# Performance work log

Hardware: AMD Instinct MI355X
Metric: run time of the kernel (lower is better)

The kernel has to match this reference:

```python
import jax, jax.numpy as jnp
import numpy as np

N = 4096
IN_F = 512
OUT_F = 256
HEADS = 4
HEAD_DIM = OUT_F // HEADS


def setup_inputs() -> dict:
    key = jax.random.key(0)
    k_feat, k_adj, k_w, k_a = jax.random.split(key, 4)
    features = jax.random.normal(k_feat, (N, IN_F), dtype=jnp.float32)
    adj_matrix = jax.random.uniform(k_adj, (N, N), dtype=jnp.float32)
    # xavier-uniform-ish init scaled small
    W = jax.random.normal(k_w, (OUT_F, IN_F), dtype=jnp.float32) * (1.0 / np.sqrt(IN_F))
    a = jax.random.normal(k_a, (HEADS, 2 * HEAD_DIM), dtype=jnp.float32) * 0.1
    bias = jnp.zeros((OUT_F,), dtype=jnp.float32)
    return {"features": features, "adj_matrix": adj_matrix, "W": W, "a": a, "bias": bias}


def reference(features, adj_matrix, W, a, bias):
    n = features.shape[0]
    h = features @ W.T                      # [N, OUT_F]
    hh = h.reshape(n, HEADS, HEAD_DIM)      # [N, H, D]
    # e[i,j,h] = leaky_relu(<h_i, a[:, :D]> + <h_j, a[:, D:]>) -- additive decomposition
    e_src = jnp.einsum('nhd,hd->nh', hh, a[:, :HEAD_DIM])   # [N, H]
    e_dst = jnp.einsum('nhd,hd->nh', hh, a[:, HEAD_DIM:])   # [N, H]
    e = e_src[:, None, :] + e_dst[None, :, :]               # [N, N, H]
    e = jnp.where(e >= 0, e, 0.2 * e)                       # leaky_relu(0.2)
    mask = adj_matrix[:, :, None] > 0.1                     # [N, N, 1]
    e = jnp.where(mask, e, -jnp.inf)
    attention = jax.nn.softmax(e, axis=1)                   # softmax over j
    attention = jnp.nan_to_num(attention, nan=0.0)          # fully-masked rows -> 0
    attention_mean = attention.mean(axis=2)                 # [N, N]
    h_out = attention_mean @ h + bias                       # [N, OUT_F]
    return h_out
```

## Files before the change

### kernel.cpp

```cpp
#include <hip/hip_runtime.h>
#include <math.h>

#define NN      4096
#define INF_    512
#define OUTF    256
#define NHEAD   4
#define HDIM    64
#define KSPLIT  8

typedef __attribute__((ext_vector_type(8))) short  short8x;
typedef __attribute__((ext_vector_type(4))) float  float4x;
typedef __attribute__((ext_vector_type(2))) float  float2x;

__device__ __forceinline__ unsigned short f2bf(float x) {
    union { float f; unsigned int u; } c; c.f = x;
    unsigned int r = (c.u + 0x7FFFu + ((c.u >> 16) & 1u)) >> 16;
    return (unsigned short)r;
}
__device__ __forceinline__ float2x bf2up(unsigned int u) {
    union { unsigned int x; float f; } lo, hi;
    lo.x = u << 16; hi.x = u & 0xFFFF0000u;
    float2x r; r[0] = lo.f; r[1] = hi.f; return r;
}
__device__ __forceinline__ float2x max2(float2x a, float2x b) {
    float2x r; r[0] = fmaxf(a[0], b[0]); r[1] = fmaxf(a[1], b[1]); return r;
}

__global__ __launch_bounds__(256) void k_cast(const float* __restrict__ feat,
                                              const float* __restrict__ W,
                                              unsigned short* __restrict__ featb,
                                              unsigned short* __restrict__ Wb) {
    const int b = blockIdx.x;
    const float* src;
    unsigned short* dst;
    int idx;
    if (b < 2048) { src = feat; dst = featb; idx = b * 1024 + threadIdx.x * 4; }
    else          { src = W;    dst = Wb;    idx = (b - 2048) * 1024 + threadIdx.x * 4; }
    float4x v = *(const float4x*)(src + idx);
    ushort4 u;
    u.x = f2bf(v[0]); u.y = f2bf(v[1]); u.z = f2bf(v[2]); u.w = f2bf(v[3]);
    *(ushort4*)(dst + idx) = u;
}

__global__ __launch_bounds__(256) void k_hedge(const unsigned short* __restrict__ featb,
                                               const unsigned short* __restrict__ Wb,
                                               const float* __restrict__ a,
                                               unsigned short* __restrict__ hT,
                                               float* __restrict__ es,
                                               unsigned short* __restrict__ Bt,
                                               unsigned short* __restrict__ Dt) {
    __shared__ __align__(16) unsigned short lds_f[64 * 40];
    __shared__ __align__(16) unsigned short lds_w[256 * 40];
    const int tid  = threadIdx.x;
    const int w    = tid >> 6;
    const int lane = tid & 63;
    const int lidx = lane & 15;
    const int quad = lane >> 4;
    const int i0   = blockIdx.x * 64;
    const int sr = tid >> 2;
    const int skq = (tid & 3) * 8;

    float4x acc[4][4];
    #pragma unroll
    for (int p = 0; p < 4; ++p)
        #pragma unroll
        for (int q = 0; q < 4; ++q)
            acc[p][q] = (float4x){0.f, 0.f, 0.f, 0.f};

    for (int kt = 0; kt < INF_; kt += 32) {
        __syncthreads();
        *(ushort4*)&lds_f[sr * 40 + skq]     = *(const ushort4*)&featb[(size_t)(i0 + sr) * INF_ + kt + skq];
        *(ushort4*)&lds_f[sr * 40 + skq + 4] = *(const ushort4*)&featb[(size_t)(i0 + sr) * INF_ + kt + skq + 4];
        #pragma unroll
        for (int itr = 0; itr < 4; ++itr) {
            int n = itr * 64 + sr;
            *(ushort4*)&lds_w[n * 40 + skq]     = *(const ushort4*)&Wb[(size_t)n * INF_ + kt + skq];
            *(ushort4*)&lds_w[n * 40 + skq + 4] = *(const ushort4*)&Wb[(size_t)n * INF_ + kt + skq + 4];
        }
        __syncthreads();
        short8x af[4], bw[4];
        #pragma unroll
        for (int t = 0; t < 4; ++t) {
            af[t] = *(const short8x*)&lds_f[(t * 16 + lidx) * 40 + quad * 8];
            bw[t] = *(const short8x*)&lds_w[(w * 64 + t * 16 + lidx) * 40 + quad * 8];
        }
        #pragma unroll
        for (int it = 0; it < 4; ++it)
            #pragma unroll
            for (int nt = 0; nt < 4; ++nt)
                acc[it][nt] = __builtin_amdgcn_mfma_f32_16x16x32_bf16(
                    af[it], bw[nt], acc[it][nt], 0, 0, 0);
    }
    #pragma unroll
    for (int it = 0; it < 4; ++it)
        #pragma unroll
        for (int nt = 0; nt < 4; ++nt) {
            int col = w * 64 + nt * 16 + lidx;
            int m0r = i0 + it * 16 + quad * 4;
            ushort4 u;
            u.x = f2bf(acc[it][nt][0]); u.y = f2bf(acc[it][nt][1]);
            u.z = f2bf(acc[it][nt][2]); u.w = f2bf(acc[it][nt][3]);
            *(ushort4*)&hT[(size_t)col * NN + m0r] = u;
        }
    float asrc[4], adst[4];
    #pragma unroll
    for (int nt = 0; nt < 4; ++nt) {
        asrc[nt] = a[w * 2 * HDIM + nt * 16 + lidx];
        adst[nt] = a[w * 2 * HDIM + HDIM + nt * 16 + lidx];
    }
    #pragma unroll
    for (int it = 0; it < 4; ++it)
        #pragma unroll
        for (int r = 0; r < 4; ++r) {
            float s = 0.f, d = 0.f;
            #pragma unroll
            for (int nt = 0; nt < 4; ++nt) {
                s += acc[it][nt][r] * asrc[nt];
                d += acc[it][nt][r] * adst[nt];
            }
            #pragma unroll
            for (int off = 1; off < 16; off <<= 1) {
                s += __shfl_xor(s, off);
                d += __shfl_xor(d, off);
            }
            if (lidx == 0) {
                int row = i0 + it * 16 + quad * 4 + r;
                es[row * NHEAD + w] = s;
                Bt[row * NHEAD + w] = f2bf(__expf(d));
                Dt[row * NHEAD + w] = f2bf(__expf(0.2f * d));
            }
        }
}

__global__ __launch_bounds__(256) void k_attn(const float* __restrict__ adj,
                                              const float* __restrict__ es,
                                              const unsigned short* __restrict__ Bt,
                                              const unsigned short* __restrict__ Dt,
                                              unsigned short* __restrict__ attn) {
    __shared__ float red[4][4];
    __shared__ float cfs[4];
    const int tid = threadIdx.x;
    const int wv  = tid >> 6;
    const int lane = tid & 63;
    const int i = blockIdx.x;

    const float4x esv = ((const float4x*)es)[i];
    float2x A01, A23, C01, C23;
    A01[0] = __expf(esv[0]); A01[1] = __expf(esv[1]);
    A23[0] = __expf(esv[2]); A23[1] = __expf(esv[3]);
    C01[0] = __expf(0.2f * esv[0]); C01[1] = __expf(0.2f * esv[1]);
    C23[0] = __expf(0.2f * esv[2]); C23[1] = __expf(0.2f * esv[3]);

    const float4x* arow4 = (const float4x*)(adj + (size_t)i * NN);
    const uint4* B4 = (const uint4*)Bt;
    const uint4* D4 = (const uint4*)Dt;

    float2x m01[4][4], m23[4][4];
    float2x den01 = (float2x){0.f, 0.f};
    float2x den23 = (float2x){0.f, 0.f};
    #pragma unroll
    for (int t = 0; t < 4; ++t) {
        int jv = t * 256 + tid;
        float4x av = arow4[jv];
        uint4 bu0 = B4[jv * 2], bu1 = B4[jv * 2 + 1];
        uint4 du0 = D4[jv * 2], du1 = D4[jv * 2 + 1];
        unsigned int bwv[8] = {bu0.x, bu0.y, bu0.z, bu0.w, bu1.x, bu1.y, bu1.z, bu1.w};
        unsigned int dwv[8] = {du0.x, du0.y, du0.z, du0.w, du1.x, du1.y, du1.z, du1.w};
        #pragma unroll
        for (int u = 0; u < 4; ++u) {
            float2x b01 = bf2up(bwv[u * 2]);
            float2x b23 = bf2up(bwv[u * 2 + 1]);
            float2x d01 = bf2up(dwv[u * 2]);
            float2x d23 = bf2up(dwv[u * 2 + 1]);
            float mf = (av[u] > 0.1f) ? 1.f : 0.f;
            float2x mf2; mf2[0] = mf; mf2[1] = mf;
            m01[t][u] = mf2 * max2(A01 * b01, C01 * d01);
            m23[t][u] = mf2 * max2(A23 * b23, C23 * d23);
            den01 += m01[t][u];
            den23 += m23[t][u];
        }
    }
    float dh[4] = {den01[0], den01[1], den23[0], den23[1]};
    #pragma unroll
    for (int off = 1; off < 64; off <<= 1) {
        #pragma unroll
        for (int h = 0; h < 4; ++h)
            dh[h] += __shfl_xor(dh[h], off);
    }
    if (lane == 0) {
        #pragma unroll
        for (int h = 0; h < 4; ++h) red[wv][h] = dh[h];
    }
    __syncthreads();
    if (tid < 4)
        cfs[tid] = red[0][tid] + red[1][tid] + red[2][tid] + red[3][tid];
    __syncthreads();
    float sc[4];
    #pragma unroll
    for (int h = 0; h < 4; ++h) {
        float den = cfs[h];
        sc[h] = den > 0.f ? 0.25f / den : 0.f;
    }

    unsigned short* orow = attn + (size_t)i * NN;
    #pragma unroll
    for (int t = 0; t < 4; ++t) {
        int jv = t * 256 + tid;
        ushort4 o;
        unsigned short* op = (unsigned short*)&o;
        #pragma unroll
        for (int u = 0; u < 4; ++u) {
            float p = sc[0] * m01[t][u][0] + sc[1] * m01[t][u][1]
                    + sc[2] * m23[t][u][0] + sc[3] * m23[t][u][1];
            op[u] = f2bf(p);
        }
        *(ushort4*)&orow[jv * 4] = o;
    }
}

__global__ __launch_bounds__(256) void k_out_gemm(const unsigned short* __restrict__ attn,
                                                  const unsigned short* __restrict__ hT,
                                                  float* __restrict__ partials) {
    __shared__ __align__(16) unsigned short lds_a[32 * 40];
    __shared__ __align__(16) unsigned short lds_h[256 * 40];
    const int tid  = threadIdx.x;
    const int w    = tid >> 6;
    const int lane = tid & 63;
    const int lidx = lane & 15;
    const int quad = lane >> 4;
    const int i0    = blockIdx.x * 32;
    const int kbase = blockIdx.y * (NN / KSPLIT);
    const int srow = tid >> 3;
    const int skq  = tid & 7;

    float4x acc[2][4];
    #pragma unroll
    for (int p = 0; p < 2; ++p)
        #pragma unroll
        for (int q = 0; q < 4; ++q)
            acc[p][q] = (float4x){0.f, 0.f, 0.f, 0.f};

    ushort4 pa, ph[8];
    pa = *(const ushort4*)&attn[(size_t)(i0 + srow) * NN + kbase + skq * 4];
    #pragma unroll
    for (int it = 0; it < 8; ++it)
        ph[it] = *(const ushort4*)&hT[(size_t)(it * 32 + srow) * NN + kbase + skq * 4];

    const int KSTEPS = (NN / KSPLIT) / 32;
    for (int ks = 0; ks < KSTEPS; ++ks) {
        __syncthreads();
        *(ushort4*)&lds_a[srow * 40 + skq * 4] = pa;
        #pragma unroll
        for (int it = 0; it < 8; ++it)
            *(ushort4*)&lds_h[(it * 32 + srow) * 40 + skq * 4] = ph[it];
        __syncthreads();
        if (ks < KSTEPS - 1) {
            const int ktn = kbase + (ks + 1) * 32;
            pa = *(const ushort4*)&attn[(size_t)(i0 + srow) * NN + ktn + skq * 4];
            #pragma unroll
            for (int it = 0; it < 8; ++it)
                ph[it] = *(const ushort4*)&hT[(size_t)(it * 32 + srow) * NN + ktn + skq * 4];
        }
        short8x af[2], bfr[4];
        #pragma unroll
        for (int t = 0; t < 2; ++t)
            af[t]  = *(const short8x*)&lds_a[(t * 16 + lidx) * 40 + quad * 8];
        #pragma unroll
        for (int t = 0; t < 4; ++t)
            bfr[t] = *(const short8x*)&lds_h[(w * 64 + t * 16 + lidx) * 40 + quad * 8];
        #pragma unroll
        for (int it = 0; it < 2; ++it)
            #pragma unroll
            for (int nt = 0; nt < 4; ++nt)
                acc[it][nt] = __builtin_amdgcn_mfma_f32_16x16x32_bf16(
                    af[it], bfr[nt], acc[it][nt], 0, 0, 0);
    }
    float* pbase = partials + (size_t)blockIdx.y * NN * OUTF;
    #pragma unroll
    for (int it = 0; it < 2; ++it)
        #pragma unroll
        for (int nt = 0; nt < 4; ++nt)
            #pragma unroll
            for (int rr = 0; rr < 4; ++rr) {
                int row = i0 + it * 16 + quad * 4 + rr;
                int col = w * 64 + nt * 16 + lidx;
                pbase[(size_t)row * OUTF + col] = acc[it][nt][rr];
            }
}

__global__ __launch_bounds__(256) void k_reduce_out(const float* __restrict__ partials,
                                                    const float* __restrict__ bias,
                                                    float* __restrict__ out) {
    const int i = blockIdx.x;
    const int n = threadIdx.x;
    float acc = bias[n];
    #pragma unroll
    for (int s = 0; s < KSPLIT; ++s)
        acc += partials[((size_t)s * NN + i) * OUTF + n];
    out[(size_t)i * OUTF + n] = acc;
}

extern "C" void kernel_launch(void* const* d_in, const int* in_sizes, int n_in,
                              void* d_out, int out_size, void* d_ws, size_t ws_size,
                              hipStream_t stream) {
    const float* feat = (const float*)d_in[0];
    const float* adj  = (const float*)d_in[1];
    const float* W    = (const float*)d_in[2];
    const float* a    = (const float*)d_in[3];
    const float* bias = (const float*)d_in[4];
    float* out = (float*)d_out;

    char* ws = (char*)d_ws;
    float*          es    = (float*)(ws + 0);
    unsigned short* Btb   = (unsigned short*)(ws + (64u << 10));
    unsigned short* Dtb   = (unsigned short*)(ws + (96u << 10));
    unsigned short* hT    = (unsigned short*)(ws + (256u << 10));
    unsigned short* attn  = (unsigned short*)(ws + (2560u << 10));
    unsigned short* featb = (unsigned short*)(ws + (2560u << 10));
    unsigned short* Wb    = (unsigned short*)(ws + (6656u << 10));
    float*          partials = (float*)(ws + (35328u << 10));

    k_cast      <<<2176,              256, 0, stream>>>(feat, W, featb, Wb);
    k_hedge     <<<64,                256, 0, stream>>>(featb, Wb, a, hT, es, Btb, Dtb);
    k_attn      <<<NN,                256, 0, stream>>>(adj, es, Btb, Dtb, attn);
    k_out_gemm  <<<dim3(128, KSPLIT), 256, 0, stream>>>(attn, hT, partials);
    k_reduce_out<<<NN,                256, 0, stream>>>(partials, bias, out);
}
```

Before: 177.9 us.

## Replace split-K partials reduction with atomic adds and halve hedge tile rows

```diff
diff --git a/kernel.cpp b/kernel.cpp
--- a/kernel.cpp
+++ b/kernel.cpp
@@ -17,6 +17,11 @@
     unsigned int r = (c.u + 0x7FFFu + ((c.u >> 16) & 1u)) >> 16;
     return (unsigned short)r;
 }
+__device__ __forceinline__ unsigned int cvtpk_bf16(float lo, float hi) {
+    unsigned int r;
+    asm("v_cvt_pk_bf16_f32 %0, %1, %2" : "=v"(r) : "v"(lo), "v"(hi));
+    return r;
+}
 __device__ __forceinline__ float2x bf2up(unsigned int u) {
     union { unsigned int x; float f; } lo, hi;
     lo.x = u << 16; hi.x = u & 0xFFFF0000u;
@@ -28,14 +33,23 @@
 
 __global__ __launch_bounds__(256) void k_cast(const float* __restrict__ feat,
                                               const float* __restrict__ W,
+                                              const float* __restrict__ bias,
                                               unsigned short* __restrict__ featb,
-                                              unsigned short* __restrict__ Wb) {
+                                              unsigned short* __restrict__ Wb,
+                                              float* __restrict__ out) {
     const int b = blockIdx.x;
+    const int tid = threadIdx.x;
+    if (b >= 2176) {
+        int idx = (b - 2176) * 1024 + tid * 4;
+        float4x bv = *(const float4x*)(bias + ((tid * 4) & 255));
+        *(float4x*)(out + idx) = bv;
+        return;
+    }
     const float* src;
     unsigned short* dst;
     int idx;
-    if (b < 2048) { src = feat; dst = featb; idx = b * 1024 + threadIdx.x * 4; }
-    else          { src = W;    dst = Wb;    idx = (b - 2048) * 1024 + threadIdx.x * 4; }
+    if (b < 2048) { src = feat; dst = featb; idx = b * 1024 + tid * 4; }
+    else          { src = W;    dst = Wb;    idx = (b - 2048) * 1024 + tid * 4; }
     float4x v = *(const float4x*)(src + idx);
     ushort4 u;
     u.x = f2bf(v[0]); u.y = f2bf(v[1]); u.z = f2bf(v[2]); u.w = f2bf(v[3]);
@@ -49,58 +63,60 @@
                                                float* __restrict__ es,
                                                unsigned short* __restrict__ Bt,
                                                unsigned short* __restrict__ Dt) {
-    __shared__ __align__(16) unsigned short lds_f[64 * 40];
+    __shared__ __align__(16) unsigned short lds_f[32 * 40];
     __shared__ __align__(16) unsigned short lds_w[256 * 40];
     const int tid  = threadIdx.x;
     const int w    = tid >> 6;
     const int lane = tid & 63;
     const int lidx = lane & 15;
     const int quad = lane >> 4;
-    const int i0   = blockIdx.x * 64;
-    const int sr = tid >> 2;
-    const int skq = (tid & 3) * 8;
-
-    float4x acc[4][4];
-    #pragma unroll
-    for (int p = 0; p < 4; ++p)
+    const int i0   = blockIdx.x * 32;
+    const int srf  = tid >> 3;
+    const int skf  = (tid & 7) * 4;
+    const int srw  = tid >> 2;
+    const int skw  = (tid & 3) * 8;
+
+    float4x acc[2][4];
+    #pragma unroll
+    for (int p = 0; p < 2; ++p)
         #pragma unroll
         for (int q = 0; q < 4; ++q)
             acc[p][q] = (float4x){0.f, 0.f, 0.f, 0.f};
 
     for (int kt = 0; kt < INF_; kt += 32) {
         __syncthreads();
-        *(ushort4*)&lds_f[sr * 40 + skq]     = *(const ushort4*)&featb[(size_t)(i0 + sr) * INF_ + kt + skq];
-        *(ushort4*)&lds_f[sr * 40 + skq + 4] = *(const ushort4*)&featb[(size_t)(i0 + sr) * INF_ + kt + skq + 4];
+        *(ushort4*)&lds_f[srf * 40 + skf] = *(const ushort4*)&featb[(size_t)(i0 + srf) * INF_ + kt + skf];
         #pragma unroll
         for (int itr = 0; itr < 4; ++itr) {
-            int n = itr * 64 + sr;
-            *(ushort4*)&lds_w[n * 40 + skq]     = *(const ushort4*)&Wb[(size_t)n * INF_ + kt + skq];
-            *(ushort4*)&lds_w[n * 40 + skq + 4] = *(const ushort4*)&Wb[(size_t)n * INF_ + kt + skq + 4];
+            int n = itr * 64 + srw;
+            *(ushort4*)&lds_w[n * 40 + skw]     = *(const ushort4*)&Wb[(size_t)n * INF_ + kt + skw];
+            *(ushort4*)&lds_w[n * 40 + skw + 4] = *(const ushort4*)&Wb[(size_t)n * INF_ + kt + skw + 4];
         }
         __syncthreads();
-        short8x af[4], bw[4];
-        #pragma unroll
-        for (int t = 0; t < 4; ++t) {
+        short8x af[2], bw[4];
+        #pragma unroll
+        for (int t = 0; t < 2; ++t)
             af[t] = *(const short8x*)&lds_f[(t * 16 + lidx) * 40 + quad * 8];
+        #pragma unroll
+        for (int t = 0; t < 4; ++t)
             bw[t] = *(const short8x*)&lds_w[(w * 64 + t * 16 + lidx) * 40 + quad * 8];
-        }
-        #pragma unroll
-        for (int it = 0; it < 4; ++it)
+        #pragma unroll
+        for (int it = 0; it < 2; ++it)
             #pragma unroll
             for (int nt = 0; nt < 4; ++nt)
                 acc[it][nt] = __builtin_amdgcn_mfma_f32_16x16x32_bf16(
                     af[it], bw[nt], acc[it][nt], 0, 0, 0);
     }
     #pragma unroll
-    for (int it = 0; it < 4; ++it)
+    for (int it = 0; it < 2; ++it)
         #pragma unroll
         for (int nt = 0; nt < 4; ++nt) {
             int col = w * 64 + nt * 16 + lidx;
             int m0r = i0 + it * 16 + quad * 4;
-            ushort4 u;
-            u.x = f2bf(acc[it][nt][0]); u.y = f2bf(acc[it][nt][1]);
-            u.z = f2bf(acc[it][nt][2]); u.w = f2bf(acc[it][nt][3]);
-            *(ushort4*)&hT[(size_t)col * NN + m0r] = u;
+            uint2 u;
+            u.x = cvtpk_bf16(acc[it][nt][0], acc[it][nt][1]);
+            u.y = cvtpk_bf16(acc[it][nt][2], acc[it][nt][3]);
+            *(uint2*)&hT[(size_t)col * NN + m0r] = u;
         }
     float asrc[4], adst[4];
     #pragma unroll
@@ -109,7 +125,7 @@
         adst[nt] = a[w * 2 * HDIM + HDIM + nt * 16 + lidx];
     }
     #pragma unroll
-    for (int it = 0; it < 4; ++it)
+    for (int it = 0; it < 2; ++it)
         #pragma unroll
         for (int r = 0; r < 4; ++r) {
             float s = 0.f, d = 0.f;
@@ -206,21 +222,22 @@
     #pragma unroll
     for (int t = 0; t < 4; ++t) {
         int jv = t * 256 + tid;
-        ushort4 o;
-        unsigned short* op = (unsigned short*)&o;
+        float pv[4];
         #pragma unroll
         for (int u = 0; u < 4; ++u) {
-            float p = sc[0] * m01[t][u][0] + sc[1] * m01[t][u][1]
-                    + sc[2] * m23[t][u][0] + sc[3] * m23[t][u][1];
-            op[u] = f2bf(p);
-        }
-        *(ushort4*)&orow[jv * 4] = o;
+            pv[u] = sc[0] * m01[t][u][0] + sc[1] * m01[t][u][1]
+                  + sc[2] * m23[t][u][0] + sc[3] * m23[t][u][1];
+        }
+        uint2 o;
+        o.x = cvtpk_bf16(pv[0], pv[1]);
+        o.y = cvtpk_bf16(pv[2], pv[3]);
+        *(uint2*)&orow[jv * 4] = o;
     }
 }
 
 __global__ __launch_bounds__(256) void k_out_gemm(const unsigned short* __restrict__ attn,
                                                   const unsigned short* __restrict__ hT,
-                                                  float* __restrict__ partials) {
+                                                  float* __restrict__ out) {
     __shared__ __align__(16) unsigned short lds_a[32 * 40];
     __shared__ __align__(16) unsigned short lds_h[256 * 40];
     const int tid  = threadIdx.x;
@@ -275,7 +292,6 @@
                 acc[it][nt] = __builtin_amdgcn_mfma_f32_16x16x32_bf16(
                     af[it], bfr[nt], acc[it][nt], 0, 0, 0);
     }
-    float* pbase = partials + (size_t)blockIdx.y * NN * OUTF;
     #pragma unroll
     for (int it = 0; it < 2; ++it)
         #pragma unroll
@@ -284,20 +300,8 @@
             for (int rr = 0; rr < 4; ++rr) {
                 int row = i0 + it * 16 + quad * 4 + rr;
                 int col = w * 64 + nt * 16 + lidx;
-                pbase[(size_t)row * OUTF + col] = acc[it][nt][rr];
+                unsafeAtomicAdd(&out[(size_t)row * OUTF + col], acc[it][nt][rr]);
             }
-}
-
-__global__ __launch_bounds__(256) void k_reduce_out(const float* __restrict__ partials,
-                                                    const float* __restrict__ bias,
-                                                    float* __restrict__ out) {
-    const int i = blockIdx.x;
-    const int n = threadIdx.x;
-    float acc = bias[n];
-    #pragma unroll
-    for (int s = 0; s < KSPLIT; ++s)
-        acc += partials[((size_t)s * NN + i) * OUTF + n];
-    out[(size_t)i * OUTF + n] = acc;
 }
 
 extern "C" void kernel_launch(void* const* d_in, const int* in_sizes, int n_in,
@@ -318,11 +322,9 @@
     unsigned short* attn  = (unsigned short*)(ws + (2560u << 10));
     unsigned short* featb = (unsigned short*)(ws + (2560u << 10));
     unsigned short* Wb    = (unsigned short*)(ws + (6656u << 10));
-    float*          partials = (float*)(ws + (35328u << 10));
-
-    k_cast      <<<2176,              256, 0, stream>>>(feat, W, featb, Wb);
-    k_hedge     <<<64,                256, 0, stream>>>(featb, Wb, a, hT, es, Btb, Dtb);
+
+    k_cast      <<<3200,              256, 0, stream>>>(feat, W, bias, featb, Wb, out);
+    k_hedge     <<<128,               256, 0, stream>>>(featb, Wb, a, hT, es, Btb, Dtb);
     k_attn      <<<NN,                256, 0, stream>>>(adj, es, Btb, Dtb, attn);
-    k_out_gemm  <<<dim3(128, KSPLIT), 256, 0, stream>>>(attn, hT, partials);
-    k_reduce_out<<<NN,                256, 0, stream>>>(partials, bias, out);
-}
+    k_out_gemm  <<<dim3(128, KSPLIT), 256, 0, stream>>>(attn, hT, out);
+}
```

Result: no change. 178.6 us (+0.4%).
